# Optimization experiments

Hardware: AMD Instinct MI355X
Metric: run time of the kernel (lower is better)

The kernel has to match this reference:

```python
import jax, jax.numpy as jnp
import numpy as np
import math

B, N, OBS, ACT = 128, 64, 128, 16
D = OBS + ACT          # obs_act_input_dim = 144
DK = 128               # obs_act_output_dim (d_k)
ENC = 128              # encoder_output_dim
FIN = 1                # final_output_dim


def setup_inputs() -> dict:
    key = jax.random.key(0)
    ks = jax.random.split(key, 8)
    s = 0.05
    return {
        "observations": jax.random.normal(ks[0], (B, N, OBS), jnp.float32),
        "policies": jax.random.uniform(ks[1], (B, N, ACT), jnp.float32),
        "actions": jax.random.uniform(ks[2], (B, N, ACT), jnp.float32),
        # torch nn.Linear weights are [out, in]
        "Wk": jax.random.normal(ks[3], (DK, D), jnp.float32) * s,
        "Wq": jax.random.normal(ks[4], (DK, D), jnp.float32) * s,
        "Wv": jax.random.normal(ks[5], (DK, D), jnp.float32) * s,
        "Wenc": jax.random.normal(ks[6], (ENC, OBS), jnp.float32) * s,
        "Wfin": jax.random.normal(ks[7], (FIN, ENC + DK), jnp.float32) * s,
    }


def reference(observations, policies, actions, Wk, Wq, Wv, Wenc, Wfin):
    b, n = observations.shape[0], observations.shape[1]
    d_k = Wk.shape[0]
    oa = jnp.concatenate([observations, actions], axis=-1)      # [B,N,D]
    op = jnp.concatenate([observations, policies], axis=-1)     # [B,N,D]
    k = oa @ Wk.T                                               # [B,N,dk]
    q = oa @ Wq.T                                               # [B,N,dk]
    # torch: bmm(q, k^T).transpose(1,2) -> scores[b,i,j] = q[b,j] . k[b,i]
    scores = jnp.einsum('bjd,bid->bij', q, k)
    w = jax.nn.sigmoid(scores / math.sqrt(d_k))                 # [B,N,N]
    Va = oa @ Wv.T                                              # [B,N,dk] value of obs||action
    Vp = op @ Wv.T                                              # [B,N,dk] value of obs||policy
    # original 5D masked combine reduces to: agg[b,i,m] = (sum_j w[b,i,j]*Va[b,j]
    #   + w[b,i,m]*(Vp[b,m]-Va[b,m])) / N  (policy substituted only where j==m)
    S = jnp.einsum('bij,bjd->bid', w, Va)                       # [B,N,dk]
    agg = (S[:, :, None, :] + w[..., None] * (Vp - Va)[:, None, :, :]) / n  # [B,N,N,dk]
    enc = observations @ Wenc.T                                 # [B,N,ENC]
    enc_rep = jnp.broadcast_to(enc[:, :, None, :], (b, n, n, enc.shape[-1]))
    node = jnp.concatenate([enc_rep, agg], axis=-1)             # [B,N,N,ENC+dk]
    value = node @ Wfin.T                                       # [B,N,N,1]
    weights5 = jnp.broadcast_to(w[:, :, None, :, None], (b, n, n, n, 1))
    return value, weights5
```

## Files before the change

### kernel.cpp

```cpp
#include <hip/hip_runtime.h>
#include <stdint.h>


#define BB 128
#define NN 64
#define OBSD 128
#define ACTD 16
#define DD 144
#define DKD 128
#define RS 168

typedef float f32x4 __attribute__((ext_vector_type(4)));
typedef short bf16x8 __attribute__((ext_vector_type(8)));

#define F_U 16384
#define F_G (F_U + 256)

__device__ __forceinline__ unsigned short bf1(float x) {
  unsigned u = __float_as_uint(x);
  return (unsigned short)((u + 0x7fffu + ((u >> 16) & 1u)) >> 16);
}
__device__ __forceinline__ unsigned int pack_bf2(float x, float y) {
  return (unsigned)bf1(x) | ((unsigned)bf1(y) << 16);
}
__device__ __forceinline__ float bf2f(unsigned short s) {
  return __uint_as_float(((unsigned)s) << 16);
}

__global__ __launch_bounds__(256) void critic_setup(
    const float* __restrict__ Wk, const float* __restrict__ Wq,
    const float* __restrict__ Wv, const float* __restrict__ Wenc,
    const float* __restrict__ Wfin, float* __restrict__ ws)
{
  const int bid = blockIdx.x, t = threadIdx.x;
  if (bid < DD) {
    const int e = bid;
    if (t < 160) {
      float acc = 0.f;
      if (t < DD) {
        float a0=0.f,a1=0.f,a2=0.f,a3=0.f;
        for (int c = 0; c < DKD; c += 4) {
          a0 += Wk[(c+0)*DD + t] * Wq[(c+0)*DD + e];
          a1 += Wk[(c+1)*DD + t] * Wq[(c+1)*DD + e];
          a2 += Wk[(c+2)*DD + t] * Wq[(c+2)*DD + e];
          a3 += Wk[(c+3)*DD + t] * Wq[(c+3)*DD + e];
        }
        acc = (a0+a1)+(a2+a3);
      }
      ((unsigned short*)ws)[e * 160 + t] = bf1(acc);
    }
  } else if (bid == DD) {
    if (t < DD) {
      float a0=0.f,a1=0.f,a2=0.f,a3=0.f;
      for (int c = 0; c < DKD; c += 4) {
        a0 += Wv[(c+0)*DD + t] * Wfin[OBSD + c + 0];
        a1 += Wv[(c+1)*DD + t] * Wfin[OBSD + c + 1];
        a2 += Wv[(c+2)*DD + t] * Wfin[OBSD + c + 2];
        a3 += Wv[(c+3)*DD + t] * Wfin[OBSD + c + 3];
      }
      ws[F_U + t] = (a0+a1)+(a2+a3);
    }
  } else {
    if (t < OBSD) {
      float a0=0.f,a1=0.f,a2=0.f,a3=0.f;
      for (int c = 0; c < 128; c += 4) {
        a0 += Wenc[(c+0)*OBSD + t] * Wfin[c + 0];
        a1 += Wenc[(c+1)*OBSD + t] * Wfin[c + 1];
        a2 += Wenc[(c+2)*OBSD + t] * Wfin[c + 2];
        a3 += Wenc[(c+3)*OBSD + t] * Wfin[c + 3];
      }
      ws[F_G + t] = (a0+a1)+(a2+a3);
    }
  }
}

__global__ __launch_bounds__(512, 2) void critic_fused(
    const float* __restrict__ obs, const float* __restrict__ pol,
    const float* __restrict__ act, const float* __restrict__ ws,
    float* __restrict__ out)
{
  __shared__ __align__(16) unsigned short s_oa[NN * RS];
  __shared__ __align__(16) unsigned short s_MT[DD * RS];
  __shared__ __align__(16) unsigned short s_dpa[NN * ACTD];
  __shared__ float s_u[DD];
  __shared__ float s_g[OBSD];
  __shared__ float s_vas[NN], s_dv[NN], s_ve[16], s_sv[16];

  unsigned short* s_T = s_MT;
  float* s_w = (float*)(s_MT + 16 * RS);

  const int tid = threadIdx.x;
  const int b = blockIdx.x >> 2;
  const int i0 = (blockIdx.x & 3) * 16;

  {
    const float4* obs4 = (const float4*)(obs + (size_t)b * NN * OBSD);
    for (int idx = tid; idx < 2048; idx += 512) {
      float4 v = obs4[idx];
      int row = idx >> 5, c4 = (idx & 31) * 4;
      *(uint2*)&s_oa[row * RS + c4] = make_uint2(pack_bf2(v.x, v.y), pack_bf2(v.z, v.w));
    }
    if (tid < 256) {
      const float4* act4 = (const float4*)(act + (size_t)b * NN * ACTD);
      const float4* pol4 = (const float4*)(pol + (size_t)b * NN * ACTD);
      float4 a = act4[tid], pp = pol4[tid];
      int row = tid >> 2, t0 = (tid & 3) * 4;
      *(uint2*)&s_oa[row * RS + OBSD + t0] = make_uint2(pack_bf2(a.x, a.y), pack_bf2(a.z, a.w));
      *(uint2*)&s_dpa[row * ACTD + t0] =
          make_uint2(pack_bf2(pp.x - a.x, pp.y - a.y), pack_bf2(pp.z - a.z, pp.w - a.w));
    } else if (tid < 512) {
      int idx = tid - 256;
      int row = idx >> 2, c4 = DD + (idx & 3) * 4;
      *(uint2*)&s_oa[row * RS + c4] = make_uint2(0u, 0u);
    }
    const uint4* mt4 = (const uint4*)ws;
    for (int idx = tid; idx < 2880; idx += 512) {
      int row = idx / 20, g4 = idx - row * 20;
      *(uint4*)&s_MT[row * RS + g4 * 8] = mt4[idx];
    }
    for (int idx = tid; idx < 288; idx += 512) {
      int row = idx >> 1, h = idx & 1;
      *(uint4*)&s_MT[row * RS + DD + h * 8] = make_uint4(0u, 0u, 0u, 0u);
    }
    if (tid < DD)            s_u[tid] = ws[F_U + tid];
    else if (tid < DD + OBSD) s_g[tid - DD] = ws[F_G + (tid - DD)];
  }
  __syncthreads();

  const int wv = tid >> 6, lane = tid & 63;
  const int m = lane & 15, q = lane >> 4;

  f32x4 accT = (f32x4){0.f, 0.f, 0.f, 0.f};
  f32x4 accT8 = (f32x4){0.f, 0.f, 0.f, 0.f};
  #pragma unroll
  for (int ks = 0; ks < 5; ++ks) {
    const int koff = ks * 32 + q * 8;
    bf16x8 a = *(const bf16x8*)&s_oa[(i0 + m) * RS + koff];
    bf16x8 bb = *(const bf16x8*)&s_MT[(wv * 16 + m) * RS + koff];
    accT = __builtin_amdgcn_mfma_f32_16x16x32_bf16(a, bb, accT, 0, 0, 0);
    if (wv == 0) {
      bf16x8 b8 = *(const bf16x8*)&s_MT[(128 + m) * RS + koff];
      accT8 = __builtin_amdgcn_mfma_f32_16x16x32_bf16(a, b8, accT8, 0, 0, 0);
    }
  }
  __syncthreads();

  #pragma unroll
  for (int r = 0; r < 4; ++r)
    s_T[(q * 4 + r) * RS + wv * 16 + m] = bf1(accT[r]);
  if (wv == 0)
    #pragma unroll
    for (int r = 0; r < 4; ++r)
      s_T[(q * 4 + r) * RS + 128 + m] = bf1(accT8[r]);
  if (tid < 32) {
    int row = tid >> 1, h = tid & 1;
    *(uint4*)&s_T[row * RS + DD + h * 8] = make_uint4(0u, 0u, 0u, 0u);
  }
  __syncthreads();

  if (wv < 4) {
    f32x4 sc = (f32x4){0.f, 0.f, 0.f, 0.f};
    #pragma unroll
    for (int ks = 0; ks < 5; ++ks) {
      const int koff = ks * 32 + q * 8;
      bf16x8 a = *(const bf16x8*)&s_T[m * RS + koff];
      bf16x8 bb = *(const bf16x8*)&s_oa[(wv * 16 + m) * RS + koff];
      sc = __builtin_amdgcn_mfma_f32_16x16x32_bf16(a, bb, sc, 0, 0, 0);
    }
    const float kk = 0.08838834764831845f;
    #pragma unroll
    for (int r = 0; r < 4; ++r)
      s_w[(q * 4 + r) * 68 + wv * 16 + m] = 1.0f / (1.0f + __expf(-sc[r] * kk));
  } else if (wv == 4) {
    float a = 0.f;
    #pragma unroll
    for (int t = 0; t < ACTD; ++t) a += bf2f(s_dpa[lane * ACTD + t]) * s_u[OBSD + t];
    s_dv[lane] = a;
  } else if (wv == 5) {
    float a = 0.f;
    for (int d = 0; d < DD; ++d) a += bf2f(s_oa[lane * RS + d]) * s_u[d];
    s_vas[lane] = a;
  } else if (wv == 6 && lane < 16) {
    float a = 0.f;
    for (int d = 0; d < OBSD; ++d) a += bf2f(s_oa[(i0 + lane) * RS + d]) * s_g[d];
    s_ve[lane] = a;
  }
  __syncthreads();

  if (tid < 16) {
    float a = 0.f;
    for (int j = 0; j < NN; ++j) a += s_w[tid * 68 + j] * s_vas[j];
    s_sv[tid] = a;
  }
  __syncthreads();

  if (tid < 256) {
    const int r = tid >> 4, m4 = (tid & 15) * 4;
    float4 v;
    v.x = s_ve[r] + (s_sv[r] + s_w[r * 68 + m4 + 0] * s_dv[m4 + 0]) * (1.0f / 64.0f);
    v.y = s_ve[r] + (s_sv[r] + s_w[r * 68 + m4 + 1] * s_dv[m4 + 1]) * (1.0f / 64.0f);
    v.z = s_ve[r] + (s_sv[r] + s_w[r * 68 + m4 + 2] * s_dv[m4 + 2]) * (1.0f / 64.0f);
    v.w = s_ve[r] + (s_sv[r] + s_w[r * 68 + m4 + 3] * s_dv[m4 + 3]) * (1.0f / 64.0f);
    *(float4*)(out + ((size_t)(b * 64 + i0 + r) * 64 + m4)) = v;
  }

  float* w5 = out + (size_t)BB * NN * NN;
  #pragma unroll 4
  for (int r = 0; r < 16; ++r) {
    const float4 wv4 = *(const float4*)&s_w[r * 68 + (tid & 15) * 4];
    float4* p4 = (float4*)(w5 + ((size_t)(b * 64 + i0 + r) << 12));
    p4[tid]       = wv4;
    p4[tid + 512] = wv4;
  }
}

extern "C" void kernel_launch(void* const* d_in, const int* in_sizes, int n_in,
                              void* d_out, int out_size, void* d_ws, size_t ws_size,
                              hipStream_t stream) {
  (void)in_sizes; (void)n_in; (void)out_size; (void)ws_size;
  const float* obs  = (const float*)d_in[0];
  const float* pol  = (const float*)d_in[1];
  const float* act  = (const float*)d_in[2];
  const float* Wk   = (const float*)d_in[3];
  const float* Wq   = (const float*)d_in[4];
  const float* Wv   = (const float*)d_in[5];
  const float* Wenc = (const float*)d_in[6];
  const float* Wfin = (const float*)d_in[7];
  float* out = (float*)d_out;
  float* ws  = (float*)d_ws;
  hipLaunchKernelGGL(critic_setup, dim3(DD + 2), dim3(256), 0, stream,
                     Wk, Wq, Wv, Wenc, Wfin, ws);
  hipLaunchKernelGGL(critic_fused, dim3(BB * 4), dim3(512), 0, stream,
                     obs, pol, act, ws, out);
}
```

Measured before the change: 165.5 us.

## Fuse weight setup into a single kernel computing Q and K per block

Removes the separate setup kernel that precomputed Wk^T·Wq and the Wv/Wenc-Wfin projections. Each block now loads Wq and Wk directly, computes Q for all 64 rows and K for its 16 rows with MFMA, and forms scores from them; u and g vectors are recomputed per block. The change drops one launch and the dependent kernel boundary, but repeats redundant weight loads and projection work in all 512 blocks and lowers occupancy to one block per CU. It also stages the weight-output stores in registers before writing.

After: 182.4 us. 10.2% more time.

```diff
diff --git a/kernel.cpp b/kernel.cpp
--- a/kernel.cpp
+++ b/kernel.cpp
@@ -9,12 +9,10 @@
 #define DD 144
 #define DKD 128
 #define RS 168
+#define RSQ 136
 
 typedef float f32x4 __attribute__((ext_vector_type(4)));
 typedef short bf16x8 __attribute__((ext_vector_type(8)));
-
-#define F_U 16384
-#define F_G (F_U + 256)
 
 __device__ __forceinline__ unsigned short bf1(float x) {
   unsigned u = __float_as_uint(x);
@@ -27,71 +25,28 @@
   return __uint_as_float(((unsigned)s) << 16);
 }
 
-__global__ __launch_bounds__(256) void critic_setup(
+__global__ __launch_bounds__(512, 1) void critic_one(
+    const float* __restrict__ obs, const float* __restrict__ pol,
+    const float* __restrict__ act,
     const float* __restrict__ Wk, const float* __restrict__ Wq,
     const float* __restrict__ Wv, const float* __restrict__ Wenc,
-    const float* __restrict__ Wfin, float* __restrict__ ws)
-{
-  const int bid = blockIdx.x, t = threadIdx.x;
-  if (bid < DD) {
-    const int e = bid;
-    if (t < 160) {
-      float acc = 0.f;
-      if (t < DD) {
-        float a0=0.f,a1=0.f,a2=0.f,a3=0.f;
-        for (int c = 0; c < DKD; c += 4) {
-          a0 += Wk[(c+0)*DD + t] * Wq[(c+0)*DD + e];
-          a1 += Wk[(c+1)*DD + t] * Wq[(c+1)*DD + e];
-          a2 += Wk[(c+2)*DD + t] * Wq[(c+2)*DD + e];
-          a3 += Wk[(c+3)*DD + t] * Wq[(c+3)*DD + e];
-        }
-        acc = (a0+a1)+(a2+a3);
-      }
-      ((unsigned short*)ws)[e * 160 + t] = bf1(acc);
-    }
-  } else if (bid == DD) {
-    if (t < DD) {
-      float a0=0.f,a1=0.f,a2=0.f,a3=0.f;
-      for (int c = 0; c < DKD; c += 4) {
-        a0 += Wv[(c+0)*DD + t] * Wfin[OBSD + c + 0];
-        a1 += Wv[(c+1)*DD + t] * Wfin[OBSD + c + 1];
-        a2 += Wv[(c+2)*DD + t] * Wfin[OBSD + c + 2];
-        a3 += Wv[(c+3)*DD + t] * Wfin[OBSD + c + 3];
-      }
-      ws[F_U + t] = (a0+a1)+(a2+a3);
-    }
-  } else {
-    if (t < OBSD) {
-      float a0=0.f,a1=0.f,a2=0.f,a3=0.f;
-      for (int c = 0; c < 128; c += 4) {
-        a0 += Wenc[(c+0)*OBSD + t] * Wfin[c + 0];
-        a1 += Wenc[(c+1)*OBSD + t] * Wfin[c + 1];
-        a2 += Wenc[(c+2)*OBSD + t] * Wfin[c + 2];
-        a3 += Wenc[(c+3)*OBSD + t] * Wfin[c + 3];
-      }
-      ws[F_G + t] = (a0+a1)+(a2+a3);
-    }
-  }
-}
-
-__global__ __launch_bounds__(512, 2) void critic_fused(
-    const float* __restrict__ obs, const float* __restrict__ pol,
-    const float* __restrict__ act, const float* __restrict__ ws,
-    float* __restrict__ out)
+    const float* __restrict__ Wfin, float* __restrict__ out)
 {
   __shared__ __align__(16) unsigned short s_oa[NN * RS];
-  __shared__ __align__(16) unsigned short s_MT[DD * RS];
-  __shared__ __align__(16) unsigned short s_dpa[NN * ACTD];
+  __shared__ __align__(16) unsigned short s_W[DKD * RS];
+  __shared__ __align__(16) unsigned short s_Q[NN * RSQ];
+  __shared__ __align__(16) unsigned short s_K[16 * RSQ];
+  __shared__ __align__(16) float s_w[16 * 68];
+  __shared__ unsigned short s_dpa[NN * ACTD];
   __shared__ float s_u[DD];
   __shared__ float s_g[OBSD];
   __shared__ float s_vas[NN], s_dv[NN], s_ve[16], s_sv[16];
 
-  unsigned short* s_T = s_MT;
-  float* s_w = (float*)(s_MT + 16 * RS);
-
   const int tid = threadIdx.x;
   const int b = blockIdx.x >> 2;
   const int i0 = (blockIdx.x & 3) * 16;
+  const int wv = tid >> 6, lane = tid & 63;
+  const int m = lane & 15, q = lane >> 4;
 
   {
     const float4* obs4 = (const float4*)(obs + (size_t)b * NN * OBSD);
@@ -113,58 +68,102 @@
       int row = idx >> 2, c4 = DD + (idx & 3) * 4;
       *(uint2*)&s_oa[row * RS + c4] = make_uint2(0u, 0u);
     }
-    const uint4* mt4 = (const uint4*)ws;
-    for (int idx = tid; idx < 2880; idx += 512) {
-      int row = idx / 20, g4 = idx - row * 20;
-      *(uint4*)&s_MT[row * RS + g4 * 8] = mt4[idx];
-    }
-    for (int idx = tid; idx < 288; idx += 512) {
-      int row = idx >> 1, h = idx & 1;
-      *(uint4*)&s_MT[row * RS + DD + h * 8] = make_uint4(0u, 0u, 0u, 0u);
-    }
-    if (tid < DD)            s_u[tid] = ws[F_U + tid];
-    else if (tid < DD + OBSD) s_g[tid - DD] = ws[F_G + (tid - DD)];
-  }
-  __syncthreads();
-
-  const int wv = tid >> 6, lane = tid & 63;
-  const int m = lane & 15, q = lane >> 4;
-
-  f32x4 accT = (f32x4){0.f, 0.f, 0.f, 0.f};
-  f32x4 accT8 = (f32x4){0.f, 0.f, 0.f, 0.f};
-  #pragma unroll
-  for (int ks = 0; ks < 5; ++ks) {
-    const int koff = ks * 32 + q * 8;
-    bf16x8 a = *(const bf16x8*)&s_oa[(i0 + m) * RS + koff];
-    bf16x8 bb = *(const bf16x8*)&s_MT[(wv * 16 + m) * RS + koff];
-    accT = __builtin_amdgcn_mfma_f32_16x16x32_bf16(a, bb, accT, 0, 0, 0);
-    if (wv == 0) {
-      bf16x8 b8 = *(const bf16x8*)&s_MT[(128 + m) * RS + koff];
-      accT8 = __builtin_amdgcn_mfma_f32_16x16x32_bf16(a, b8, accT8, 0, 0, 0);
-    }
-  }
-  __syncthreads();
-
-  #pragma unroll
-  for (int r = 0; r < 4; ++r)
-    s_T[(q * 4 + r) * RS + wv * 16 + m] = bf1(accT[r]);
-  if (wv == 0)
+    const float4* W4 = (const float4*)Wq;
+    for (int idx = tid; idx < 4608; idx += 512) {
+      int row = idx / 36, g4 = idx - row * 36;
+      float4 v = W4[idx];
+      *(uint2*)&s_W[row * RS + g4 * 4] = make_uint2(pack_bf2(v.x, v.y), pack_bf2(v.z, v.w));
+    }
+    for (int idx = tid; idx < 512; idx += 512) {
+      int row = idx >> 2, c4 = DD + (idx & 3) * 4;
+      *(uint2*)&s_W[row * RS + c4] = make_uint2(0u, 0u);
+    }
+    if (tid < DD) {
+      float a0=0.f,a1=0.f,a2=0.f,a3=0.f,a4=0.f,a5=0.f,a6=0.f,a7=0.f;
+      for (int c = 0; c < DKD; c += 8) {
+        a0 += Wv[(c+0)*DD + tid] * Wfin[OBSD + c + 0];
+        a1 += Wv[(c+1)*DD + tid] * Wfin[OBSD + c + 1];
+        a2 += Wv[(c+2)*DD + tid] * Wfin[OBSD + c + 2];
+        a3 += Wv[(c+3)*DD + tid] * Wfin[OBSD + c + 3];
+        a4 += Wv[(c+4)*DD + tid] * Wfin[OBSD + c + 4];
+        a5 += Wv[(c+5)*DD + tid] * Wfin[OBSD + c + 5];
+        a6 += Wv[(c+6)*DD + tid] * Wfin[OBSD + c + 6];
+        a7 += Wv[(c+7)*DD + tid] * Wfin[OBSD + c + 7];
+      }
+      s_u[tid] = ((a0+a1)+(a2+a3)) + ((a4+a5)+(a6+a7));
+    } else if (tid < DD + OBSD) {
+      const int d = tid - DD;
+      float a0=0.f,a1=0.f,a2=0.f,a3=0.f,a4=0.f,a5=0.f,a6=0.f,a7=0.f;
+      for (int c = 0; c < 128; c += 8) {
+        a0 += Wenc[(c+0)*OBSD + d] * Wfin[c + 0];
+        a1 += Wenc[(c+1)*OBSD + d] * Wfin[c + 1];
+        a2 += Wenc[(c+2)*OBSD + d] * Wfin[c + 2];
+        a3 += Wenc[(c+3)*OBSD + d] * Wfin[c + 3];
+        a4 += Wenc[(c+4)*OBSD + d] * Wfin[c + 4];
+        a5 += Wenc[(c+5)*OBSD + d] * Wfin[c + 5];
+        a6 += Wenc[(c+6)*OBSD + d] * Wfin[c + 6];
+        a7 += Wenc[(c+7)*OBSD + d] * Wfin[c + 7];
+      }
+      s_g[d] = ((a0+a1)+(a2+a3)) + ((a4+a5)+(a6+a7));
+    }
+  }
+  __syncthreads();
+
+  {
+    const int jt = wv & 3, n0 = (wv >> 2) * 4;
+    f32x4 acc[4];
+    #pragma unroll
+    for (int t = 0; t < 4; ++t) acc[t] = (f32x4){0.f, 0.f, 0.f, 0.f};
+    #pragma unroll
+    for (int ks = 0; ks < 5; ++ks) {
+      const int koff = ks * 32 + q * 8;
+      bf16x8 a = *(const bf16x8*)&s_oa[(jt * 16 + m) * RS + koff];
+      #pragma unroll
+      for (int t = 0; t < 4; ++t) {
+        bf16x8 bb = *(const bf16x8*)&s_W[((n0 + t) * 16 + m) * RS + koff];
+        acc[t] = __builtin_amdgcn_mfma_f32_16x16x32_bf16(a, bb, acc[t], 0, 0, 0);
+      }
+    }
+    #pragma unroll
+    for (int t = 0; t < 4; ++t)
+      #pragma unroll
+      for (int r = 0; r < 4; ++r)
+        s_Q[(jt * 16 + q * 4 + r) * RSQ + (n0 + t) * 16 + m] = bf1(acc[t][r]);
+  }
+  __syncthreads();
+
+  {
+    const float4* W4 = (const float4*)Wk;
+    for (int idx = tid; idx < 4608; idx += 512) {
+      int row = idx / 36, g4 = idx - row * 36;
+      float4 v = W4[idx];
+      *(uint2*)&s_W[row * RS + g4 * 4] = make_uint2(pack_bf2(v.x, v.y), pack_bf2(v.z, v.w));
+    }
+  }
+  __syncthreads();
+
+  {
+    f32x4 acc = (f32x4){0.f, 0.f, 0.f, 0.f};
+    #pragma unroll
+    for (int ks = 0; ks < 5; ++ks) {
+      const int koff = ks * 32 + q * 8;
+      bf16x8 a = *(const bf16x8*)&s_oa[(i0 + m) * RS + koff];
+      bf16x8 bb = *(const bf16x8*)&s_W[(wv * 16 + m) * RS + koff];
+      acc = __builtin_amdgcn_mfma_f32_16x16x32_bf16(a, bb, acc, 0, 0, 0);
+    }
     #pragma unroll
     for (int r = 0; r < 4; ++r)
-      s_T[(q * 4 + r) * RS + 128 + m] = bf1(accT8[r]);
-  if (tid < 32) {
-    int row = tid >> 1, h = tid & 1;
-    *(uint4*)&s_T[row * RS + DD + h * 8] = make_uint4(0u, 0u, 0u, 0u);
+      s_K[(q * 4 + r) * RSQ + wv * 16 + m] = bf1(acc[r]);
   }
   __syncthreads();
 
   if (wv < 4) {
     f32x4 sc = (f32x4){0.f, 0.f, 0.f, 0.f};
     #pragma unroll
-    for (int ks = 0; ks < 5; ++ks) {
+    for (int ks = 0; ks < 4; ++ks) {
       const int koff = ks * 32 + q * 8;
-      bf16x8 a = *(const bf16x8*)&s_T[m * RS + koff];
-      bf16x8 bb = *(const bf16x8*)&s_oa[(wv * 16 + m) * RS + koff];
+      bf16x8 a = *(const bf16x8*)&s_K[m * RSQ + koff];
+      bf16x8 bb = *(const bf16x8*)&s_Q[(wv * 16 + m) * RSQ + koff];
       sc = __builtin_amdgcn_mfma_f32_16x16x32_bf16(a, bb, sc, 0, 0, 0);
     }
     const float kk = 0.08838834764831845f;
@@ -204,20 +203,23 @@
     *(float4*)(out + ((size_t)(b * 64 + i0 + r) * 64 + m4)) = v;
   }
 
+  float4 wr[16];
+  #pragma unroll
+  for (int r = 0; r < 16; ++r)
+    wr[r] = *(const float4*)&s_w[r * 68 + (tid & 15) * 4];
   float* w5 = out + (size_t)BB * NN * NN;
-  #pragma unroll 4
+  #pragma unroll
   for (int r = 0; r < 16; ++r) {
-    const float4 wv4 = *(const float4*)&s_w[r * 68 + (tid & 15) * 4];
     float4* p4 = (float4*)(w5 + ((size_t)(b * 64 + i0 + r) << 12));
-    p4[tid]       = wv4;
-    p4[tid + 512] = wv4;
+    p4[tid]       = wr[r];
+    p4[tid + 512] = wr[r];
   }
 }
 
 extern "C" void kernel_launch(void* const* d_in, const int* in_sizes, int n_in,
                               void* d_out, int out_size, void* d_ws, size_t ws_size,
                               hipStream_t stream) {
-  (void)in_sizes; (void)n_in; (void)out_size; (void)ws_size;
+  (void)in_sizes; (void)n_in; (void)out_size; (void)d_ws; (void)ws_size;
   const float* obs  = (const float*)d_in[0];
   const float* pol  = (const float*)d_in[1];
   const float* act  = (const float*)d_in[2];
@@ -227,9 +229,6 @@
   const float* Wenc = (const float*)d_in[6];
   const float* Wfin = (const float*)d_in[7];
   float* out = (float*)d_out;
-  float* ws  = (float*)d_ws;
-  hipLaunchKernelGGL(critic_setup, dim3(DD + 2), dim3(256), 0, stream,
-                     Wk, Wq, Wv, Wenc, Wfin, ws);
-  hipLaunchKernelGGL(critic_fused, dim3(BB * 4), dim3(512), 0, stream,
-                     obs, pol, act, ws, out);
-}
+  hipLaunchKernelGGL(critic_one, dim3(BB * 4), dim3(512), 0, stream,
+                     obs, pol, act, Wk, Wq, Wv, Wenc, Wfin, out);
+}
```
